# Kernel tuning notes

Measured on AMD Instinct MI355X. Metric: run time of the kernel, lower is better.

## Reference

```python
import jax, jax.numpy as jnp
import numpy as np

R = 3.0            # search_range
EPS = 0.01         # forward_backward_error
UPD_MULT = 1.0     # UPDATE_MULTIPLIER_THRESHOLD


def _clamp(coords, H, W):
    # coords [..., 2] = (x, y); clamp x to [0, W-1], y to [0, H-1]
    return jnp.stack([jnp.clip(coords[..., 0], 0.0, W - 1.0),
                      jnp.clip(coords[..., 1], 0.0, H - 1.0)], axis=-1)


def _scores(coords, corr_flat):
    # coords [B,H,W,2] (x,y); corr_flat [B*H*W, Hc, Wc]; bilinear sample one scalar per pixel
    B, H, W, _ = coords.shape
    N, Hc, Wc = corr_flat.shape
    c = coords.reshape(-1, 2)
    x, y = c[:, 0], c[:, 1]
    x0 = jnp.floor(x); y0 = jnp.floor(y)
    wx = x - x0; wy = y - y0
    x0i = jnp.clip(x0.astype(jnp.int32), 0, Wc - 1)
    x1i = jnp.clip(x0i + 1, 0, Wc - 1)
    y0i = jnp.clip(y0.astype(jnp.int32), 0, Hc - 1)
    y1i = jnp.clip(y0i + 1, 0, Hc - 1)
    n = jnp.arange(N)
    v00 = corr_flat[n, y0i, x0i]; v01 = corr_flat[n, y0i, x1i]
    v10 = corr_flat[n, y1i, x0i]; v11 = corr_flat[n, y1i, x1i]
    s = (v00 * (1 - wx) * (1 - wy) + v01 * wx * (1 - wy)
         + v10 * (1 - wx) * wy + v11 * wx * wy)
    return s.reshape(B, H, W)


def _propagate(coords, corr_flat, dxy):
    # PatchMatch propagation step along direction (dx, dy): take neighbor's match
    # shifted by the same pixel offset if it scores higher.
    dx, dy = dxy
    B, H, W, _ = coords.shape
    best = coords
    best_s = _scores(best, corr_flat)
    cand_h = _clamp(jnp.roll(coords, dx, axis=2) + jnp.array([dx, 0.0], coords.dtype), H, W)
    cand_v = _clamp(jnp.roll(coords, dy, axis=1) + jnp.array([0.0, dy], coords.dtype), H, W)
    for cand in (cand_h, cand_v):
        s = _scores(cand, corr_flat)
        upd = s > best_s
        best = jnp.where(upd[..., None], cand, best)
        best_s = jnp.maximum(s, best_s)
    return best


def _random_search(coords, corr_flat, key):
    B, H, W, _ = coords.shape
    new = _clamp(coords + R * jax.random.normal(key, coords.shape, coords.dtype), H, W)
    old_s = _scores(coords, corr_flat)
    new_s = _scores(new, corr_flat)
    upd = (new_s - UPD_MULT * old_s) > 0
    return jnp.where(upd[..., None], new, coords)


def _handle(matching, corr_flat, key):
    coords = jnp.transpose(matching, (0, 2, 3, 1))  # [B,H,W,2]
    k1, k2, k3 = jax.random.split(key, 3)
    res = _propagate(coords, corr_flat, (1, 1))
    res = _random_search(res, corr_flat, k1)
    res = _propagate(res, corr_flat, (-1, -1))
    res = _random_search(res, corr_flat, k2)
    res = _propagate(res, corr_flat, (-1, 1))
    res = _random_search(res, corr_flat, k3)
    res = _propagate(res, corr_flat, (1, -1))
    return res


def _bilinear_map(img, coords):
    # img [B,H,W,C] sampled at coords [B,H,W,2] (x,y) -> [B,H,W,C]
    B, H, W, C = img.shape
    def per_b(im, co):
        x = co[..., 0].reshape(-1); y = co[..., 1].reshape(-1)
        x0 = jnp.floor(x); y0 = jnp.floor(y)
        wx = (x - x0)[:, None]; wy = (y - y0)[:, None]
        x0i = jnp.clip(x0.astype(jnp.int32), 0, W - 1)
        x1i = jnp.clip(x0i + 1, 0, W - 1)
        y0i = jnp.clip(y0.astype(jnp.int32), 0, H - 1)
        y1i = jnp.clip(y0i + 1, 0, H - 1)
        v00 = im[y0i, x0i]; v01 = im[y0i, x1i]
        v10 = im[y1i, x0i]; v11 = im[y1i, x1i]
        out = (v00 * (1 - wx) * (1 - wy) + v01 * wx * (1 - wy)
               + v10 * (1 - wx) * wy + v11 * wx * wy)
        return out.reshape(H, W, C)
    return jax.vmap(per_b)(img, coords)


def setup_inputs() -> dict:
    key = jax.random.key(0)
    k1, k2, k3 = jax.random.split(key, 3)
    B, H, W = 4, 64, 64
    # matching fields: absolute (x, y) coords in-range
    mf = jax.random.uniform(k1, (B, 2, H, W), jnp.float32)
    mb = jax.random.uniform(k2, (B, 2, H, W), jnp.float32)
    scale = jnp.array([W - 1.0, H - 1.0], jnp.float32).reshape(1, 2, 1, 1)
    matching_f = mf * scale
    matching_b = mb * scale
    corr_map = jax.random.normal(k3, (B, H, W, H, W), jnp.float32)
    return {"matching_f": matching_f, "matching_b": matching_b, "corr_map": corr_map}


def reference(matching_f, matching_b, corr_map):
    B, H, W = corr_map.shape[0], corr_map.shape[1], corr_map.shape[2]
    corr_f = corr_map.reshape(B * H * W, H, W)
    # backward direction samples the transposed correlation volume
    corr_b = jnp.transpose(corr_map, (0, 3, 4, 1, 2)).reshape(B * H * W, H, W)
    key = jax.random.key(42)
    kf, kb = jax.random.split(key)
    res_f = _handle(matching_f, corr_f, kf)   # [B,H,W,2]
    res_b = _handle(matching_b, corr_b, kb)   # [B,H,W,2]
    # forward-backward consistency: sample backward field at forward matches
    counter = _bilinear_map(res_b, res_f)
    diff = jnp.max(jnp.abs(res_f - counter), axis=-1)
    invalid = (diff > EPS)[..., None]
    res = jnp.where(invalid, jnp.transpose(matching_f, (0, 2, 3, 1)), res_f)
    return jnp.transpose(res, (0, 3, 1, 2))
```

## Files before the change

### kernel.cpp

```cpp
#include <hip/hip_runtime.h>
#include <stdint.h>

#pragma clang fp contract(off)

__host__ __device__ inline void tf2x32(uint32_t k0, uint32_t k1,
                                       uint32_t x0, uint32_t x1,
                                       uint32_t* o0, uint32_t* o1) {
  const uint32_t ks2 = k0 ^ k1 ^ 0x1BD11BDAu;
  x0 += k0; x1 += k1;
#define TF_R(r) { x0 += x1; x1 = (x1 << (r)) | (x1 >> (32 - (r))); x1 ^= x0; }
  TF_R(13) TF_R(15) TF_R(26) TF_R(6)
  x0 += k1;  x1 += ks2 + 1u;
  TF_R(17) TF_R(29) TF_R(16) TF_R(24)
  x0 += ks2; x1 += k0 + 2u;
  TF_R(13) TF_R(15) TF_R(26) TF_R(6)
  x0 += k0;  x1 += k1 + 3u;
  TF_R(17) TF_R(29) TF_R(16) TF_R(24)
  x0 += k1;  x1 += ks2 + 4u;
  TF_R(13) TF_R(15) TF_R(26) TF_R(6)
  x0 += ks2; x1 += k0 + 5u;
#undef TF_R
  *o0 = x0; *o1 = x1;
}

__device__ inline float erfinv_xla(float x) {
#pragma clang fp contract(off)
  float w = -log1pf(-(x * x));
  float p;
  if (w < 5.0f) {
    w = w - 2.5f;
    p = 2.81022636e-08f;
    p = 3.43273939e-07f  + p * w;
    p = -3.5233877e-06f  + p * w;
    p = -4.39150654e-06f + p * w;
    p = 0.00021858087f   + p * w;
    p = -0.00125372503f  + p * w;
    p = -0.00417768164f  + p * w;
    p = 0.246640727f     + p * w;
    p = 1.50140941f      + p * w;
  } else {
    w = sqrtf(w) - 3.0f;
    p = -0.000200214257f;
    p = 0.000100950558f  + p * w;
    p = 0.00134934322f   + p * w;
    p = -0.00367342844f  + p * w;
    p = 0.00573950773f   + p * w;
    p = -0.0076224613f   + p * w;
    p = 0.00943887047f   + p * w;
    p = 1.00167406f      + p * w;
    p = 2.83297682f      + p * w;
  }
  return p * x;
}

__device__ inline float jax_normal(uint32_t k0, uint32_t k1, uint32_t idx) {
#pragma clang fp contract(off)
  uint32_t o0, o1;
  tf2x32(k0, k1, 0u, idx, &o0, &o1);
  uint32_t bits = o0 ^ o1;
  float f = __uint_as_float((bits >> 9) | 0x3f800000u) - 1.0f;
  float u = f * 2.0f + (-0x1.fffffep-1f);
  u = fmaxf(-0x1.fffffep-1f, u);
  return 0x1.6a09e6p+0f * erfinv_xla(u);
}

__device__ inline float score_at(const float* __restrict__ base, int stride,
                                 float x, float y) {
#pragma clang fp contract(off)
  float x0 = floorf(x), y0 = floorf(y);
  float wx = x - x0, wy = y - y0;
  int xi = (int)x0; xi = xi < 0 ? 0 : (xi > 63 ? 63 : xi);
  int yi = (int)y0; yi = yi < 0 ? 0 : (yi > 63 ? 63 : yi);
  int x1 = xi + 1 > 63 ? 63 : xi + 1;
  int y1 = yi + 1 > 63 ? 63 : yi + 1;
  float v00 = base[(yi * 64 + xi) * stride];
  float v01 = base[(yi * 64 + x1) * stride];
  float v10 = base[(y1 * 64 + xi) * stride];
  float v11 = base[(y1 * 64 + x1) * stride];
  float omx = 1.0f - wx, omy = 1.0f - wy;
  return (((v00 * omx) * omy + (v01 * wx) * omy) + (v10 * omx) * wy) + (v11 * wx) * wy;
}

__global__ __launch_bounds__(64) void step_kernel(
    const float* __restrict__ mf, const float* __restrict__ mb,
    const float4* __restrict__ in_c, float4* __restrict__ out_c,
    const float* __restrict__ corr, int dx, int dy,
    uint32_t k0f, uint32_t k1f, uint32_t k0b, uint32_t k1b,
    int do_rs, int from_matching) {
#pragma clang fp contract(off)
  int g = (int)(blockIdx.x * 64 + threadIdx.x);
  int dir = g >> 14, b = (g >> 12) & 3, p = g & 4095;
  int i = p >> 6, j = p & 63;

  const float* base; int stride;
  if (dir == 0) { base = corr + (size_t)(b * 4096 + p) * 4096; stride = 1; }
  else          { base = corr + (size_t)b * 16777216 + p;      stride = 4096; }

  int jh = (j - dx) & 63;
  int iv = (i - dy) & 63;

  float2 bst; float bs;
  float2 ch, cv;
  if (from_matching) {
    const float* m = dir ? mb : mf;
    float2 c = make_float2(m[((b * 2 + 0) * 64 + i) * 64 + j],
                           m[((b * 2 + 1) * 64 + i) * 64 + j]);
    ch = make_float2(m[((b * 2 + 0) * 64 + i ) * 64 + jh], m[((b * 2 + 1) * 64 + i ) * 64 + jh]);
    cv = make_float2(m[((b * 2 + 0) * 64 + iv) * 64 + j ], m[((b * 2 + 1) * 64 + iv) * 64 + j ]);
    bst = c;
    bs = score_at(base, stride, c.x, c.y);
  } else {
    const float4* ic = in_c + dir * 16384 + b * 4096;
    float4 own = ic[p];
    float4 nh  = ic[(i << 6) | jh];
    float4 nv  = ic[(iv << 6) | j];
    bst = make_float2(own.x, own.y);
    bs  = own.z;
    ch = make_float2(nh.x, nh.y);
    cv = make_float2(nv.x, nv.y);
  }
  ch.x = fminf(fmaxf(ch.x + (float)dx, 0.0f), 63.0f);
  cv.y = fminf(fmaxf(cv.y + (float)dy, 0.0f), 63.0f);

  float sh = score_at(base, stride, ch.x, ch.y);
  float sv = score_at(base, stride, cv.x, cv.y);
  if (sh > bs) bst = ch;
  bs = fmaxf(sh, bs);
  if (sv > bs) bst = cv;
  bs = fmaxf(sv, bs);

  if (do_rs) {
    uint32_t kk0 = dir ? k0b : k0f, kk1 = dir ? k1b : k1f;
    uint32_t pg = (uint32_t)(b * 4096 + p);
    float n0 = jax_normal(kk0, kk1, 2u * pg);
    float n1 = jax_normal(kk0, kk1, 2u * pg + 1u);
    float nx = fminf(fmaxf(bst.x + 3.0f * n0, 0.0f), 63.0f);
    float ny = fminf(fmaxf(bst.y + 3.0f * n1, 0.0f), 63.0f);
    float sn = score_at(base, stride, nx, ny);
    if (sn - bs > 0.0f) { bst = make_float2(nx, ny); bs = sn; }
  }
  out_c[dir * 16384 + b * 4096 + p] = make_float4(bst.x, bst.y, bs, 0.0f);
}

__global__ __launch_bounds__(256) void combine_kernel(const float* __restrict__ mf,
                                                      const float4* __restrict__ res,
                                                      float* __restrict__ out) {
#pragma clang fp contract(off)
  int pg = (int)(blockIdx.x * 256 + threadIdx.x);
  int b = pg >> 12, hw = pg & 4095;
  int i = hw >> 6, j = hw & 63;
  float4 rf4 = res[pg];
  float2 rf = make_float2(rf4.x, rf4.y);
  const float4* rb = res + 16384 + b * 4096;
  float x0 = floorf(rf.x), y0 = floorf(rf.y);
  float wx = rf.x - x0, wy = rf.y - y0;
  int xi = (int)x0; xi = xi < 0 ? 0 : (xi > 63 ? 63 : xi);
  int yi = (int)y0; yi = yi < 0 ? 0 : (yi > 63 ? 63 : yi);
  int x1 = xi + 1 > 63 ? 63 : xi + 1;
  int y1 = yi + 1 > 63 ? 63 : yi + 1;
  float4 v00 = rb[yi * 64 + xi], v01 = rb[yi * 64 + x1];
  float4 v10 = rb[y1 * 64 + xi], v11 = rb[y1 * 64 + x1];
  float omx = 1.0f - wx, omy = 1.0f - wy;
  float c0 = (((v00.x * omx) * omy + (v01.x * wx) * omy) + (v10.x * omx) * wy) + (v11.x * wx) * wy;
  float c1 = (((v00.y * omx) * omy + (v01.y * wx) * omy) + (v10.y * omx) * wy) + (v11.y * wx) * wy;
  float d = fmaxf(fabsf(rf.x - c0), fabsf(rf.y - c1));
  bool invalid = d > 0.01f;
  out[((b * 2 + 0) * 64 + i) * 64 + j] = invalid ? mf[((b * 2 + 0) * 64 + i) * 64 + j] : rf.x;
  out[((b * 2 + 1) * 64 + i) * 64 + j] = invalid ? mf[((b * 2 + 1) * 64 + i) * 64 + j] : rf.y;
}

extern "C" void kernel_launch(void* const* d_in, const int* in_sizes, int n_in,
                              void* d_out, int out_size, void* d_ws, size_t ws_size,
                              hipStream_t stream) {
  const float* mf   = (const float*)d_in[0];
  const float* mb   = (const float*)d_in[1];
  const float* corr = (const float*)d_in[2];
  float* out  = (float*)d_out;
  float4* bufA = (float4*)d_ws;
  float4* bufB = bufA + 32768;

  uint32_t kf0, kf1, kb0, kb1, K[12];
  tf2x32(0u, 42u, 0u, 0u, &kf0, &kf1);
  tf2x32(0u, 42u, 0u, 1u, &kb0, &kb1);
  for (uint32_t s = 0; s < 3; ++s) {
    tf2x32(kf0, kf1, 0u, s, &K[0 + s * 2], &K[0 + s * 2 + 1]);
    tf2x32(kb0, kb1, 0u, s, &K[6 + s * 2], &K[6 + s * 2 + 1]);
  }

  dim3 grid(512), block(64);
  step_kernel<<<grid, block, 0, stream>>>(mf, mb, nullptr, bufA, corr,  1,  1,
                                          K[0], K[1], K[6], K[7], 1, 1);
  step_kernel<<<grid, block, 0, stream>>>(mf, mb, bufA, bufB, corr, -1, -1,
                                          K[2], K[3], K[8], K[9], 1, 0);
  step_kernel<<<grid, block, 0, stream>>>(mf, mb, bufB, bufA, corr, -1,  1,
                                          K[4], K[5], K[10], K[11], 1, 0);
  step_kernel<<<grid, block, 0, stream>>>(mf, mb, bufA, bufB, corr,  1, -1,
                                          0u, 0u, 0u, 0u, 0, 0);
  combine_kernel<<<dim3(64), dim3(256), 0, stream>>>(mf, bufB, out);
  (void)in_sizes; (void)n_in; (void)out_size; (void)ws_size;
}
```

Before: 333.5 us.

## Fuse final propagation step into combine kernel, recomputing backward step at sample points

```diff
diff --git a/kernel.cpp b/kernel.cpp
--- a/kernel.cpp
+++ b/kernel.cpp
@@ -86,7 +86,7 @@
     const float4* __restrict__ in_c, float4* __restrict__ out_c,
     const float* __restrict__ corr, int dx, int dy,
     uint32_t k0f, uint32_t k1f, uint32_t k0b, uint32_t k1b,
-    int do_rs, int from_matching) {
+    int from_matching) {
 #pragma clang fp contract(off)
   int g = (int)(blockIdx.x * 64 + threadIdx.x);
   int dir = g >> 14, b = (g >> 12) & 3, p = g & 4095;
@@ -129,37 +129,77 @@
   if (sv > bs) bst = cv;
   bs = fmaxf(sv, bs);
 
-  if (do_rs) {
-    uint32_t kk0 = dir ? k0b : k0f, kk1 = dir ? k1b : k1f;
-    uint32_t pg = (uint32_t)(b * 4096 + p);
-    float n0 = jax_normal(kk0, kk1, 2u * pg);
-    float n1 = jax_normal(kk0, kk1, 2u * pg + 1u);
-    float nx = fminf(fmaxf(bst.x + 3.0f * n0, 0.0f), 63.0f);
-    float ny = fminf(fmaxf(bst.y + 3.0f * n1, 0.0f), 63.0f);
-    float sn = score_at(base, stride, nx, ny);
-    if (sn - bs > 0.0f) { bst = make_float2(nx, ny); bs = sn; }
-  }
+  uint32_t kk0 = dir ? k0b : k0f, kk1 = dir ? k1b : k1f;
+  uint32_t pg = (uint32_t)(b * 4096 + p);
+  float n0 = jax_normal(kk0, kk1, 2u * pg);
+  float n1 = jax_normal(kk0, kk1, 2u * pg + 1u);
+  float nx = fminf(fmaxf(bst.x + 3.0f * n0, 0.0f), 63.0f);
+  float ny = fminf(fmaxf(bst.y + 3.0f * n1, 0.0f), 63.0f);
+  float sn = score_at(base, stride, nx, ny);
+  if (sn - bs > 0.0f) { bst = make_float2(nx, ny); bs = sn; }
+
   out_c[dir * 16384 + b * 4096 + p] = make_float4(bst.x, bst.y, bs, 0.0f);
 }
 
-__global__ __launch_bounds__(256) void combine_kernel(const float* __restrict__ mf,
-                                                      const float4* __restrict__ res,
-                                                      float* __restrict__ out) {
-#pragma clang fp contract(off)
-  int pg = (int)(blockIdx.x * 256 + threadIdx.x);
-  int b = pg >> 12, hw = pg & 4095;
-  int i = hw >> 6, j = hw & 63;
-  float4 rf4 = res[pg];
-  float2 rf = make_float2(rf4.x, rf4.y);
-  const float4* rb = res + 16384 + b * 4096;
+__global__ __launch_bounds__(64) void step4_combine_kernel(
+    const float* __restrict__ mf, const float4* __restrict__ in_c,
+    const float* __restrict__ corr, float* __restrict__ out) {
+#pragma clang fp contract(off)
+  int pg = (int)(blockIdx.x * 64 + threadIdx.x);
+  int b = pg >> 12, p = pg & 4095;
+  int i = p >> 6, j = p & 63;
+
+  float2 rf;
+  {
+    const float* base = corr + (size_t)(b * 4096 + p) * 4096;
+    const float4* ic = in_c + b * 4096;
+    float4 own = ic[p];
+    int jh = (j - 1) & 63, iv = (i + 1) & 63;
+    float4 nh = ic[(i << 6) | jh];
+    float4 nv = ic[(iv << 6) | j];
+    float2 ch = make_float2(fminf(fmaxf(nh.x + 1.0f, 0.0f), 63.0f), nh.y);
+    float2 cv = make_float2(nv.x, fminf(fmaxf(nv.y - 1.0f, 0.0f), 63.0f));
+    float sh = score_at(base, 1, ch.x, ch.y);
+    float sv = score_at(base, 1, cv.x, cv.y);
+    float2 bst = make_float2(own.x, own.y); float bs = own.z;
+    if (sh > bs) bst = ch;
+    bs = fmaxf(sh, bs);
+    if (sv > bs) bst = cv;
+    rf = bst;
+  }
+
   float x0 = floorf(rf.x), y0 = floorf(rf.y);
   float wx = rf.x - x0, wy = rf.y - y0;
   int xi = (int)x0; xi = xi < 0 ? 0 : (xi > 63 ? 63 : xi);
   int yi = (int)y0; yi = yi < 0 ? 0 : (yi > 63 ? 63 : yi);
   int x1 = xi + 1 > 63 ? 63 : xi + 1;
   int y1 = yi + 1 > 63 ? 63 : yi + 1;
-  float4 v00 = rb[yi * 64 + xi], v01 = rb[yi * 64 + x1];
-  float4 v10 = rb[y1 * 64 + xi], v11 = rb[y1 * 64 + x1];
+
+  const float4* ic1 = in_c + 16384 + b * 4096;
+  const float* cb = corr + (size_t)b * 16777216;
+  auto step4_b = [&](int ci, int cj) -> float2 {
+#pragma clang fp contract(off)
+    int q = (ci << 6) | cj;
+    const float* base = cb + q;
+    float4 own = ic1[q];
+    int jh = (cj - 1) & 63, iv = (ci + 1) & 63;
+    float4 nh = ic1[(ci << 6) | jh];
+    float4 nv = ic1[(iv << 6) | cj];
+    float2 ch = make_float2(fminf(fmaxf(nh.x + 1.0f, 0.0f), 63.0f), nh.y);
+    float2 cv = make_float2(nv.x, fminf(fmaxf(nv.y - 1.0f, 0.0f), 63.0f));
+    float sh = score_at(base, 4096, ch.x, ch.y);
+    float sv = score_at(base, 4096, cv.x, cv.y);
+    float2 bst = make_float2(own.x, own.y); float bs = own.z;
+    if (sh > bs) bst = ch;
+    bs = fmaxf(sh, bs);
+    if (sv > bs) bst = cv;
+    return bst;
+  };
+  float2 v00 = step4_b(yi, xi);
+  float2 v01 = step4_b(yi, x1);
+  float2 v10 = step4_b(y1, xi);
+  float2 v11 = step4_b(y1, x1);
+
   float omx = 1.0f - wx, omy = 1.0f - wy;
   float c0 = (((v00.x * omx) * omy + (v01.x * wx) * omy) + (v10.x * omx) * wy) + (v11.x * wx) * wy;
   float c1 = (((v00.y * omx) * omy + (v01.y * wx) * omy) + (v10.y * omx) * wy) + (v11.y * wx) * wy;
@@ -189,13 +229,11 @@
 
   dim3 grid(512), block(64);
   step_kernel<<<grid, block, 0, stream>>>(mf, mb, nullptr, bufA, corr,  1,  1,
-                                          K[0], K[1], K[6], K[7], 1, 1);
+                                          K[0], K[1], K[6], K[7], 1);
   step_kernel<<<grid, block, 0, stream>>>(mf, mb, bufA, bufB, corr, -1, -1,
-                                          K[2], K[3], K[8], K[9], 1, 0);
+                                          K[2], K[3], K[8], K[9], 0);
   step_kernel<<<grid, block, 0, stream>>>(mf, mb, bufB, bufA, corr, -1,  1,
-                                          K[4], K[5], K[10], K[11], 1, 0);
-  step_kernel<<<grid, block, 0, stream>>>(mf, mb, bufA, bufB, corr,  1, -1,
-                                          0u, 0u, 0u, 0u, 0, 0);
-  combine_kernel<<<dim3(64), dim3(256), 0, stream>>>(mf, bufB, out);
+                                          K[4], K[5], K[10], K[11], 0);
+  step4_combine_kernel<<<dim3(256), dim3(64), 0, stream>>>(mf, bufA, corr, out);
   (void)in_sizes; (void)n_in; (void)out_size; (void)ws_size;
 }
```

New measurement: 335.0 us. Within noise of the previous version (+0.4%).
